# Kernel optimization log

Hardware: AMD Instinct MI355X
Metric: run time of the kernel (lower is better)

Reference implementation:

```python
import math
import jax, jax.numpy as jnp
import numpy as np

B, CI, CO, K, WD, H = 8, 512, 512, 3, 512, 64


def setup_inputs() -> dict:
    key = jax.random.key(0)
    ks = jax.random.split(key, 8)
    x = jax.random.normal(ks[0], (B, CI, H, H), jnp.float32)
    style = jax.random.normal(ks[1], (B, WD), jnp.float32)
    noise = jax.random.normal(ks[2], (B, CO, H, H), jnp.float32)
    # learned params
    weight = jax.random.normal(ks[3], (1, CO, CI, K, K), jnp.float32)      # ModulatedConv2d.weight
    mod_weight = jax.random.normal(ks[4], (CI, WD), jnp.float32)            # EqualLinear.weight
    mod_bias = jnp.ones((CI,), jnp.float32)                                  # bias_init=1
    noise_weight = 0.1 * jnp.ones((1,), jnp.float32)                         # NoiseInjection.weight (nonzero for signal)
    act_bias = 0.01 * jax.random.normal(ks[5], (CO,), jnp.float32)           # FusedLeakyReLU.bias
    return {"x": x, "style": style, "noise": noise, "weight": weight,
            "mod_weight": mod_weight, "mod_bias": mod_bias,
            "noise_weight": noise_weight, "act_bias": act_bias}


def reference(x, style, noise, weight, mod_weight, mod_bias, noise_weight, act_bias):
    # EqualLinear modulation: scale = 1/sqrt(w_space_dim), lr_mul = 1
    eq_scale = 1.0 / math.sqrt(WD)
    s = style @ (mod_weight * eq_scale).T + mod_bias            # [B, CI]
    # modulate + demodulate per-sample weights
    conv_scale = 1.0 / math.sqrt(CI * K * K)                     # 1/sqrt(fan_in)
    w = conv_scale * weight * s[:, None, :, None, None]          # [B, CO, CI, K, K]
    demod = jax.lax.rsqrt(jnp.sum(w * w, axis=(2, 3, 4)) + 1e-8)  # [B, CO]
    w = w * demod[:, :, None, None, None]
    pad = K // 2

    def conv1(xi, wi):  # per-sample conv (equivalent to groups=batch trick)
        return jax.lax.conv_general_dilated(
            xi[None], wi, window_strides=(1, 1),
            padding=[(pad, pad), (pad, pad)],
            dimension_numbers=("NCHW", "OIHW", "NCHW"))[0]

    out = jax.vmap(conv1)(x, w)                                  # [B, CO, H, H]
    # noise injection (noise provided -> no normalization branch)
    out = out + noise_weight[0] * noise
    # fused leaky relu: leaky_relu(out + bias) * sqrt(2)
    out = jax.nn.leaky_relu(out + act_bias[None, :, None, None], 0.2) * math.sqrt(2.0)
    return out
```

## Files before the change

kernel.cpp:

```cpp
#include <hip/hip_runtime.h>
#include <hip/hip_bf16.h>

typedef unsigned short u16;
typedef unsigned long long u64;
typedef short bf16x8 __attribute__((ext_vector_type(8)));
typedef float f32x4 __attribute__((ext_vector_type(4)));

#define EQ_SCALE   0.04419417382415922f
#define CONV_SCALE 0.014731391274719738f

#define WS_S   0
#define WS_ESC (16*1024)
#define WS_WSQ (32*1024)
#define WS_WT  (32*1024 + 1024*1024)
#define WS_XS  (WS_WT + 9*512*512*2)
#define WS_Z   (WS_XS + 8*64*64*512*2)

__device__ __forceinline__ void gld16(void* l, const void* g) {
  __builtin_amdgcn_global_load_lds((const __attribute__((address_space(1))) void*)g,
                                   (__attribute__((address_space(3))) void*)l,
                                   16, 0, 0);
}

__device__ __forceinline__ u16 f2b_rne(float f) {
  union { float f; unsigned int i; } c; c.f = f;
  unsigned int r = (c.i + 0x7FFFu + ((c.i >> 16) & 1u)) >> 16;
  return (u16)r;
}

__global__ void k_style(const float* __restrict__ style, const float* __restrict__ mw,
                        const float* __restrict__ mb, float* __restrict__ s) {
  int g = blockIdx.x * 4 + (threadIdx.x >> 6);
  int lane = threadIdx.x & 63;
  int b = g >> 9, i = g & 511;
  const float4* sr = (const float4*)(style + (b << 9));
  const float4* wr = (const float4*)(mw + (i << 9));
  float acc = 0.f;
#pragma unroll
  for (int j = 0; j < 2; ++j) {
    float4 a = sr[lane * 2 + j];
    float4 w4 = wr[lane * 2 + j];
    acc += a.x * w4.x + a.y * w4.y + a.z * w4.z + a.w * w4.w;
  }
#pragma unroll
  for (int off = 32; off; off >>= 1) acc += __shfl_xor(acc, off);
  if (lane == 0) s[g] = acc * EQ_SCALE + mb[i];
}

__global__ void k_wsq(const float* __restrict__ w, float* __restrict__ wsq) {
  int idx = blockIdx.x * 256 + threadIdx.x;
  const float* p = w + idx * 9;
  float a = 0.f;
  for (int t = 0; t < 9; ++t) { float v = p[t]; a += v * v; }
  wsq[idx] = a;
}

__global__ void k_esc(const float* __restrict__ wsq, const float* __restrict__ s,
                      float* __restrict__ esc) {
  int g = blockIdx.x * 4 + (threadIdx.x >> 6);
  int lane = threadIdx.x & 63;
  int b = g >> 9, o = g & 511;
  const float4* wr = (const float4*)(wsq + (o << 9));
  const float4* sr = (const float4*)(s + (b << 9));
  float a = 0.f;
#pragma unroll
  for (int j = 0; j < 2; ++j) {
    float4 wv = wr[lane * 2 + j];
    float4 sv = sr[lane * 2 + j];
    a += wv.x * sv.x * sv.x + wv.y * sv.y * sv.y + wv.z * sv.z * sv.z + wv.w * sv.w * sv.w;
  }
#pragma unroll
  for (int off = 32; off; off >>= 1) a += __shfl_xor(a, off);
  if (lane == 0) esc[g] = CONV_SCALE * rsqrtf(CONV_SCALE * CONV_SCALE * a + 1e-8f);
}

__global__ void k_zero(u64* __restrict__ z) {
  z[blockIdx.x * 256 + threadIdx.x] = 0ull;
}

__global__ void k_wt(const float* __restrict__ w, u16* __restrict__ wt) {
  int idx = blockIdx.x * 256 + threadIdx.x;
  const float* p = w + idx * 9;
  for (int t = 0; t < 9; ++t) wt[t * 262144 + idx] = f2b_rne(p[t]);
}

__global__ void k_xs(const float* __restrict__ x, const float* __restrict__ s,
                     u16* __restrict__ xs) {
  __shared__ u16 tile[64 * 66];
  int by = blockIdx.x;
  int i0 = blockIdx.y << 6;
  int b = by >> 6, y = by & 63;
  int t = threadIdx.x, w = t >> 6, lane = t & 63;
  for (int k = 0; k < 16; ++k) {
    int il = w + (k << 2);
    int i = i0 + il;
    float v = x[((((b << 9) + i) << 6) | y) << 6 | lane] * s[(b << 9) + i];
    tile[lane * 66 + il] = f2b_rne(v);
  }
  __syncthreads();
  for (int k = 0; k < 16; ++k) {
    int xc = w + (k << 2);
    xs[((((b << 6) | y) << 6 | xc) << 9) + i0 + lane] = tile[xc * 66 + lane];
  }
}

__global__ void __launch_bounds__(512, 1) k_conv(
    const u16* __restrict__ wt, const u16* __restrict__ xs,
    const u16* __restrict__ zbuf,
    const float* __restrict__ esc, const float* __restrict__ noise,
    const float* __restrict__ nwp, const float* __restrict__ abias,
    float* __restrict__ out) {
  __shared__ __align__(16) u16 ldsA[2][128 * 64];
  __shared__ __align__(16) u16 ldsB[2][384 * 64];

  const int t = threadIdx.x;
  const int w = t >> 6, lane = t & 63;
  const int wm = w >> 2, wrw = w & 3;
  const int quad = lane >> 4, l15 = lane & 15;

  const int flat = blockIdx.y * 4 + blockIdx.x;
  const int xcd = flat & 7, rest = flat >> 3;
  const int o0 = (xcd & 3) << 7;
  const int nt = (rest << 1) | (xcd >> 2);
  const int b = nt >> 4, y0 = (nt & 15) << 2;

  const u16* bgp[6];
#pragma unroll
  for (int j = 0; j < 6; ++j) {
    int c = j * 512 + t;
    int pos = c >> 3, swz = c & 7;
    int ci16 = swz ^ (pos & 7);
    int col = pos & 63;
    int yy = y0 - 1 + j;
    if ((unsigned)yy < 64u)
      bgp[j] = xs + ((((b << 6) + yy) << 6) + col) * 512 + ci16 * 8;
    else
      bgp[j] = zbuf + col * 512 + ci16 * 8;
  }
  int agOff[2];
#pragma unroll
  for (int j = 0; j < 2; ++j) {
    int c = j * 512 + t;
    int ol = c >> 3, swz = c & 7;
    int ci16 = swz ^ (ol & 7);
    agOff[j] = (o0 + ol) * 512 + ci16 * 8;
  }

  f32x4 acc[16];
#pragma unroll
  for (int i = 0; i < 16; ++i) acc[i] = (f32x4)0.f;

  int aBase[4], aXor[4];
#pragma unroll
  for (int mf = 0; mf < 4; ++mf) {
    int ol = wm * 64 + mf * 16 + l15;
    aBase[mf] = ol * 8;
    aXor[mf] = ol & 7;
  }

#pragma unroll
  for (int j = 0; j < 6; ++j)
    gld16(&ldsB[0][(j * 512 + w * 64) * 8], bgp[j]);
#pragma unroll
  for (int j = 0; j < 2; ++j)
    gld16(&ldsA[0][(j * 512 + w * 64) * 8], wt + agOff[j]);

#pragma unroll 1
  for (int cib = 0; cib < 8; ++cib) {
    const u16* bR = &ldsB[cib & 1][0];
#pragma unroll
    for (int khw = 0; khw < 9; ++khw) {
      if (khw == 7) { asm volatile("s_waitcnt vmcnt(6)" ::: "memory"); }
      else         { asm volatile("s_waitcnt vmcnt(0)" ::: "memory"); }
      __builtin_amdgcn_s_barrier();
      __builtin_amdgcn_sched_barrier(0);

      const int par = (cib + khw) & 1;
      const u16* aR = &ldsA[par][0];

      {
        u16* aW = (u16*)&ldsA[par ^ 1][0];
        const int nkhw = (khw == 8) ? 0 : khw + 1;
        const int ncib = (khw == 8) ? ((cib + 1) & 7) : cib;
#pragma unroll
        for (int j = 0; j < 2; ++j)
          gld16(aW + (j * 512 + w * 64) * 8,
                wt + agOff[j] + nkhw * 262144 + ncib * 64);
      }
      if (khw == 6) {
        u16* bW = (u16*)&ldsB[(cib & 1) ^ 1][0];
        const int pc = (cib + 1) & 7;
#pragma unroll
        for (int j = 0; j < 6; ++j)
          gld16(bW + (j * 512 + w * 64) * 8, bgp[j] + pc * 64);
      }

      const int kh = khw / 3, kw = khw % 3;
      const int tr = wrw + kh;
      int bBase[4], bXor[4];
      unsigned cmask[4];
#pragma unroll
      for (int nf = 0; nf < 4; ++nf) {
        int ci = nf * 16 + l15 + kw - 1;
        cmask[nf] = ((kw == 0 && nf == 0) || (kw == 2 && nf == 3))
                        ? (unsigned)((unsigned)ci > 63u) : 0u;
        ci &= 63;
        int pos = tr * 64 + ci;
        bBase[nf] = pos * 8;
        bXor[nf] = pos & 7;
      }
#pragma unroll
      for (int ks = 0; ks < 2; ++ks) {
        const int kci = ks * 4 + quad;
        bf16x8 af[4], bv[4];
#pragma unroll
        for (int mf = 0; mf < 4; ++mf)
          af[mf] = *(const bf16x8*)(aR + (aBase[mf] + (kci ^ aXor[mf])) * 8);
#pragma unroll
        for (int nf = 0; nf < 4; ++nf) {
          bf16x8 v = *(const bf16x8*)(bR + (bBase[nf] + (kci ^ bXor[nf])) * 8);
          bf16x8 z = {0, 0, 0, 0, 0, 0, 0, 0};
          bv[nf] = cmask[nf] ? z : v;
        }
        __builtin_amdgcn_s_setprio(1);
#pragma unroll
        for (int mf = 0; mf < 4; ++mf)
#pragma unroll
          for (int nf = 0; nf < 4; ++nf)
            acc[mf * 4 + nf] = __builtin_amdgcn_mfma_f32_16x16x32_bf16(
                af[mf], bv[nf], acc[mf * 4 + nf], 0, 0, 0);
        __builtin_amdgcn_s_setprio(0);
      }
    }
  }
  asm volatile("s_waitcnt vmcnt(0)" ::: "memory");

  const float nwv = nwp[0];
  const int y = y0 + wrw;
#pragma unroll
  for (int mf = 0; mf < 4; ++mf) {
#pragma unroll
    for (int r = 0; r < 4; ++r) {
      int o = o0 + wm * 64 + mf * 16 + quad * 4 + r;
      float es = esc[(b << 9) + o];
      float ab = abias[o];
      int rowbase = ((((b << 9) + o) << 6) | y) << 6;
#pragma unroll
      for (int nf = 0; nf < 4; ++nf) {
        int col = nf * 16 + l15;
        int idx = rowbase | col;
        float v = acc[mf * 4 + nf][r] * es + nwv * noise[idx] + ab;
        v = (v < 0.f ? 0.2f * v : v) * 1.4142135623730951f;
        out[idx] = v;
      }
    }
  }
}

extern "C" void kernel_launch(void* const* d_in, const int* in_sizes, int n_in,
                              void* d_out, int out_size, void* d_ws, size_t ws_size,
                              hipStream_t stream) {
  const float* x      = (const float*)d_in[0];
  const float* style  = (const float*)d_in[1];
  const float* noise  = (const float*)d_in[2];
  const float* weight = (const float*)d_in[3];
  const float* mw     = (const float*)d_in[4];
  const float* mb     = (const float*)d_in[5];
  const float* nw     = (const float*)d_in[6];
  const float* ab     = (const float*)d_in[7];
  float* out = (float*)d_out;

  char* ws = (char*)d_ws;
  float* s   = (float*)(ws + WS_S);
  float* esc = (float*)(ws + WS_ESC);
  float* wsq = (float*)(ws + WS_WSQ);
  u16* wt    = (u16*)(ws + WS_WT);
  u16* xs    = (u16*)(ws + WS_XS);
  u16* zbuf  = (u16*)(ws + WS_Z);

  k_zero<<<32, 256, 0, stream>>>((u64*)zbuf);
  k_style<<<1024, 256, 0, stream>>>(style, mw, mb, s);
  k_wsq<<<1024, 256, 0, stream>>>(weight, wsq);
  k_esc<<<1024, 256, 0, stream>>>(wsq, s, esc);
  k_wt<<<1024, 256, 0, stream>>>(weight, wt);
  k_xs<<<dim3(512, 8), 256, 0, stream>>>(x, s, xs);
  k_conv<<<dim3(4, 128), 512, 0, stream>>>(wt, xs, zbuf, esc, noise, nw, ab, out);
}
```

Measured before the change: 365.0 us.

## Double conv output-channel tile to 256 and merge preprocessing kernels into two launches

The conv kernel now computes 256 output channels per block instead of 128. Each wave holds 32 accumulators, and the grid drops to 256 blocks, so each staged input tile is reused across more MFMAs and fewer redundant B loads are made. The six preprocessing kernels are merged into two launches, dispatched by block index, which cuts launch overhead. The cost is doubled LDS for A and higher register pressure. With 256 blocks on 256 CUs, occupancy and load balance become tighter.

```diff
diff --git a/kernel.cpp b/kernel.cpp
--- a/kernel.cpp
+++ b/kernel.cpp
@@ -28,78 +28,82 @@
   return (u16)r;
 }
 
-__global__ void k_style(const float* __restrict__ style, const float* __restrict__ mw,
-                        const float* __restrict__ mb, float* __restrict__ s) {
-  int g = blockIdx.x * 4 + (threadIdx.x >> 6);
-  int lane = threadIdx.x & 63;
+__global__ void __launch_bounds__(256) k_pre1(
+    const float* __restrict__ style, const float* __restrict__ mw,
+    const float* __restrict__ mb, const float* __restrict__ w,
+    float* __restrict__ s, float* __restrict__ wsq, u64* __restrict__ z) {
+  int bid = blockIdx.x, t = threadIdx.x;
+  if (bid < 32) { z[bid * 256 + t] = 0ull; return; }
+  if (bid < 1056) {
+    int idx = (bid - 32) * 256 + t;
+    const float* p = w + idx * 9;
+    float a = 0.f;
+#pragma unroll
+    for (int k = 0; k < 9; ++k) { float v = p[k]; a += v * v; }
+    wsq[idx] = a;
+    return;
+  }
+  int g = (bid - 1056) * 4 + (t >> 6);
+  int lane = t & 63;
   int b = g >> 9, i = g & 511;
   const float4* sr = (const float4*)(style + (b << 9));
   const float4* wr = (const float4*)(mw + (i << 9));
   float acc = 0.f;
 #pragma unroll
   for (int j = 0; j < 2; ++j) {
-    float4 a = sr[lane * 2 + j];
+    float4 a4 = sr[lane * 2 + j];
     float4 w4 = wr[lane * 2 + j];
-    acc += a.x * w4.x + a.y * w4.y + a.z * w4.z + a.w * w4.w;
+    acc += a4.x * w4.x + a4.y * w4.y + a4.z * w4.z + a4.w * w4.w;
   }
 #pragma unroll
   for (int off = 32; off; off >>= 1) acc += __shfl_xor(acc, off);
   if (lane == 0) s[g] = acc * EQ_SCALE + mb[i];
 }
 
-__global__ void k_wsq(const float* __restrict__ w, float* __restrict__ wsq) {
-  int idx = blockIdx.x * 256 + threadIdx.x;
-  const float* p = w + idx * 9;
-  float a = 0.f;
-  for (int t = 0; t < 9; ++t) { float v = p[t]; a += v * v; }
-  wsq[idx] = a;
-}
-
-__global__ void k_esc(const float* __restrict__ wsq, const float* __restrict__ s,
-                      float* __restrict__ esc) {
-  int g = blockIdx.x * 4 + (threadIdx.x >> 6);
-  int lane = threadIdx.x & 63;
-  int b = g >> 9, o = g & 511;
-  const float4* wr = (const float4*)(wsq + (o << 9));
-  const float4* sr = (const float4*)(s + (b << 9));
-  float a = 0.f;
-#pragma unroll
-  for (int j = 0; j < 2; ++j) {
-    float4 wv = wr[lane * 2 + j];
-    float4 sv = sr[lane * 2 + j];
-    a += wv.x * sv.x * sv.x + wv.y * sv.y * sv.y + wv.z * sv.z * sv.z + wv.w * sv.w * sv.w;
-  }
-#pragma unroll
-  for (int off = 32; off; off >>= 1) a += __shfl_xor(a, off);
-  if (lane == 0) esc[g] = CONV_SCALE * rsqrtf(CONV_SCALE * CONV_SCALE * a + 1e-8f);
-}
-
-__global__ void k_zero(u64* __restrict__ z) {
-  z[blockIdx.x * 256 + threadIdx.x] = 0ull;
-}
-
-__global__ void k_wt(const float* __restrict__ w, u16* __restrict__ wt) {
-  int idx = blockIdx.x * 256 + threadIdx.x;
-  const float* p = w + idx * 9;
-  for (int t = 0; t < 9; ++t) wt[t * 262144 + idx] = f2b_rne(p[t]);
-}
-
-__global__ void k_xs(const float* __restrict__ x, const float* __restrict__ s,
-                     u16* __restrict__ xs) {
+__global__ void __launch_bounds__(256) k_pre2(
+    const float* __restrict__ wsq, const float* __restrict__ s,
+    const float* __restrict__ w, const float* __restrict__ x,
+    float* __restrict__ esc, u16* __restrict__ wt, u16* __restrict__ xs) {
   __shared__ u16 tile[64 * 66];
-  int by = blockIdx.x;
-  int i0 = blockIdx.y << 6;
+  int bid = blockIdx.x, t = threadIdx.x;
+  if (bid < 1024) {
+    int g = bid * 4 + (t >> 6);
+    int lane = t & 63;
+    int b = g >> 9, o = g & 511;
+    const float4* wr = (const float4*)(wsq + (o << 9));
+    const float4* sr = (const float4*)(s + (b << 9));
+    float a = 0.f;
+#pragma unroll
+    for (int j = 0; j < 2; ++j) {
+      float4 wv = wr[lane * 2 + j];
+      float4 sv = sr[lane * 2 + j];
+      a += wv.x*sv.x*sv.x + wv.y*sv.y*sv.y + wv.z*sv.z*sv.z + wv.w*sv.w*sv.w;
+    }
+#pragma unroll
+    for (int off = 32; off; off >>= 1) a += __shfl_xor(a, off);
+    if (lane == 0) esc[g] = CONV_SCALE * rsqrtf(CONV_SCALE * CONV_SCALE * a + 1e-8f);
+    return;
+  }
+  if (bid < 2048) {
+    int idx = (bid - 1024) * 256 + t;
+    const float* p = w + idx * 9;
+#pragma unroll
+    for (int k = 0; k < 9; ++k) wt[k * 262144 + idx] = f2b_rne(p[k]);
+    return;
+  }
+  int v = bid - 2048;
+  int by = v & 511, i0 = (v >> 9) << 6;
   int b = by >> 6, y = by & 63;
-  int t = threadIdx.x, w = t >> 6, lane = t & 63;
+  int wv = t >> 6, lane = t & 63;
   for (int k = 0; k < 16; ++k) {
-    int il = w + (k << 2);
+    int il = wv + (k << 2);
     int i = i0 + il;
-    float v = x[((((b << 9) + i) << 6) | y) << 6 | lane] * s[(b << 9) + i];
-    tile[lane * 66 + il] = f2b_rne(v);
+    float val = x[((((b << 9) + i) << 6) | y) << 6 | lane] * s[(b << 9) + i];
+    tile[lane * 66 + il] = f2b_rne(val);
   }
   __syncthreads();
   for (int k = 0; k < 16; ++k) {
-    int xc = w + (k << 2);
+    int xc = wv + (k << 2);
     xs[((((b << 6) | y) << 6 | xc) << 9) + i0 + lane] = tile[xc * 66 + lane];
   }
 }
@@ -110,7 +114,7 @@
     const float* __restrict__ esc, const float* __restrict__ noise,
     const float* __restrict__ nwp, const float* __restrict__ abias,
     float* __restrict__ out) {
-  __shared__ __align__(16) u16 ldsA[2][128 * 64];
+  __shared__ __align__(16) u16 ldsA[2][256 * 64];
   __shared__ __align__(16) u16 ldsB[2][384 * 64];
 
   const int t = threadIdx.x;
@@ -118,10 +122,10 @@
   const int wm = w >> 2, wrw = w & 3;
   const int quad = lane >> 4, l15 = lane & 15;
 
-  const int flat = blockIdx.y * 4 + blockIdx.x;
+  const int flat = blockIdx.y * 2 + blockIdx.x;
   const int xcd = flat & 7, rest = flat >> 3;
-  const int o0 = (xcd & 3) << 7;
-  const int nt = (rest << 1) | (xcd >> 2);
+  const int o0 = (xcd >> 2) << 8;
+  const int nt = (rest << 2) | (xcd & 3);
   const int b = nt >> 4, y0 = (nt & 15) << 2;
 
   const u16* bgp[6];
@@ -137,32 +141,27 @@
     else
       bgp[j] = zbuf + col * 512 + ci16 * 8;
   }
-  int agOff[2];
-#pragma unroll
-  for (int j = 0; j < 2; ++j) {
+  int agOff[4];
+#pragma unroll
+  for (int j = 0; j < 4; ++j) {
     int c = j * 512 + t;
     int ol = c >> 3, swz = c & 7;
     int ci16 = swz ^ (ol & 7);
     agOff[j] = (o0 + ol) * 512 + ci16 * 8;
   }
 
-  f32x4 acc[16];
-#pragma unroll
-  for (int i = 0; i < 16; ++i) acc[i] = (f32x4)0.f;
-
-  int aBase[4], aXor[4];
-#pragma unroll
-  for (int mf = 0; mf < 4; ++mf) {
-    int ol = wm * 64 + mf * 16 + l15;
-    aBase[mf] = ol * 8;
-    aXor[mf] = ol & 7;
-  }
+  f32x4 acc[32];
+#pragma unroll
+  for (int i = 0; i < 32; ++i) acc[i] = (f32x4)0.f;
+
+  const int aBase0 = wm * 1024 + l15 * 8;
+  const int aXorS = l15 & 7;
 
 #pragma unroll
   for (int j = 0; j < 6; ++j)
     gld16(&ldsB[0][(j * 512 + w * 64) * 8], bgp[j]);
 #pragma unroll
-  for (int j = 0; j < 2; ++j)
+  for (int j = 0; j < 4; ++j)
     gld16(&ldsA[0][(j * 512 + w * 64) * 8], wt + agOff[j]);
 
 #pragma unroll 1
@@ -183,7 +182,7 @@
         const int nkhw = (khw == 8) ? 0 : khw + 1;
         const int ncib = (khw == 8) ? ((cib + 1) & 7) : cib;
 #pragma unroll
-        for (int j = 0; j < 2; ++j)
+        for (int j = 0; j < 4; ++j)
           gld16(aW + (j * 512 + w * 64) * 8,
                 wt + agOff[j] + nkhw * 262144 + ncib * 64);
       }
@@ -212,10 +211,10 @@
 #pragma unroll
       for (int ks = 0; ks < 2; ++ks) {
         const int kci = ks * 4 + quad;
-        bf16x8 af[4], bv[4];
-#pragma unroll
-        for (int mf = 0; mf < 4; ++mf)
-          af[mf] = *(const bf16x8*)(aR + (aBase[mf] + (kci ^ aXor[mf])) * 8);
+        bf16x8 af[8], bv[4];
+#pragma unroll
+        for (int mf = 0; mf < 8; ++mf)
+          af[mf] = *(const bf16x8*)(aR + (aBase0 + mf * 128 + (kci ^ aXorS)) * 8);
 #pragma unroll
         for (int nf = 0; nf < 4; ++nf) {
           bf16x8 v = *(const bf16x8*)(bR + (bBase[nf] + (kci ^ bXor[nf])) * 8);
@@ -224,7 +223,7 @@
         }
         __builtin_amdgcn_s_setprio(1);
 #pragma unroll
-        for (int mf = 0; mf < 4; ++mf)
+        for (int mf = 0; mf < 8; ++mf)
 #pragma unroll
           for (int nf = 0; nf < 4; ++nf)
             acc[mf * 4 + nf] = __builtin_amdgcn_mfma_f32_16x16x32_bf16(
@@ -238,10 +237,10 @@
   const float nwv = nwp[0];
   const int y = y0 + wrw;
 #pragma unroll
-  for (int mf = 0; mf < 4; ++mf) {
+  for (int mf = 0; mf < 8; ++mf) {
 #pragma unroll
     for (int r = 0; r < 4; ++r) {
-      int o = o0 + wm * 64 + mf * 16 + quad * 4 + r;
+      int o = o0 + wm * 128 + mf * 16 + quad * 4 + r;
       float es = esc[(b << 9) + o];
       float ab = abias[o];
       int rowbase = ((((b << 9) + o) << 6) | y) << 6;
@@ -278,11 +277,7 @@
   u16* xs    = (u16*)(ws + WS_XS);
   u16* zbuf  = (u16*)(ws + WS_Z);
 
-  k_zero<<<32, 256, 0, stream>>>((u64*)zbuf);
-  k_style<<<1024, 256, 0, stream>>>(style, mw, mb, s);
-  k_wsq<<<1024, 256, 0, stream>>>(weight, wsq);
-  k_esc<<<1024, 256, 0, stream>>>(wsq, s, esc);
-  k_wt<<<1024, 256, 0, stream>>>(weight, wt);
-  k_xs<<<dim3(512, 8), 256, 0, stream>>>(x, s, xs);
-  k_conv<<<dim3(4, 128), 512, 0, stream>>>(wt, xs, zbuf, esc, noise, nw, ab, out);
-}
+  k_pre1<<<2080, 256, 0, stream>>>(style, mw, mb, weight, s, wsq, (u64*)zbuf);
+  k_pre2<<<6144, 256, 0, stream>>>(wsq, s, weight, x, esc, wt, xs);
+  k_conv<<<dim3(2, 128), 512, 0, stream>>>(wt, xs, zbuf, esc, noise, nw, ab, out);
+}
```

New measurement: 353.1 us. -3.3%, faster.
